# Kernel tuning notes

Measured on AMD Instinct MI355X. Metric: run time of the kernel, lower is better.

Reference implementation:

```python
import jax, jax.numpy as jnp
import numpy as np

B, S, D = 16, 2048, 1024
FF = 4 * D
ST, EN = 0, 512          # target_dims['start'], target_dims['end']
DT = EN - ST             # intervened subspace dim


def setup_inputs() -> dict:
    key = jax.random.key(0)
    k = jax.random.split(key, 6)
    hidden_states = jax.random.normal(k[0], (B, S, D), dtype=jnp.float32)
    eot_indices = jax.random.randint(k[1], (B,), 0, S)
    scale = 0.02
    W1 = jax.random.normal(k[2], (D, FF), dtype=jnp.float32) * scale
    W2 = jax.random.normal(k[3], (FF, D), dtype=jnp.float32) * scale
    W_rot = jax.random.normal(k[4], (DT, DT), dtype=jnp.float32) * scale
    W_inv = jax.random.normal(k[5], (DT, DT), dtype=jnp.float32) * scale
    return {"hidden_states": hidden_states, "W1": W1, "W2": W2,
            "W_rot": W_rot, "W_inv": W_inv, "eot_indices": eot_indices}


def reference(hidden_states, W1, W2, W_rot, W_inv, eot_indices):
    # layers[0]: transformer FFN block (stand-in for the wrapped encoder layer)
    h = jax.nn.gelu(hidden_states @ W1) @ W2          # [B, S, D]
    b = jnp.arange(h.shape[0])
    # LinearLayer branch: gather per-example eot row, slice target subspace
    rows = h[b, eot_indices]                          # [B, D]
    target = rows[:, ST:EN]                           # [B, DT]
    # LinearLayer -> InverseLinearLayer: rotate then un-rotate the subspace
    intervention = (target @ W_rot) @ W_inv           # [B, DT]
    # scatter/replace back into the flattened hidden states (vectorized form
    # of the per-example flatten/slice/cat/stack loop in the original code)
    new_rows = rows.at[:, ST:EN].set(intervention)    # [B, D]
    reps = h.at[b, eot_indices].set(new_rows)         # [B, S, D]
    return reps
```

## Files before the change

### kernel.cpp

```cpp
#include <hip/hip_runtime.h>
#include <hip/hip_bf16.h>
#include <stdint.h>

#define B_SZ  16
#define S_SZ  2048
#define D_SZ  1024
#define FF_SZ 4096
#define DT_SZ 512

typedef __bf16 bf16x8 __attribute__((ext_vector_type(8)));
typedef float  f32x4  __attribute__((ext_vector_type(4)));
typedef short  short8 __attribute__((ext_vector_type(8)));

__device__ __forceinline__ short f2bf(float x) {
    union { float f; uint32_t u; } v; v.f = x;
    uint32_t r = (v.u + 0x7fffu + ((v.u >> 16) & 1u)) >> 16;
    return (short)(uint16_t)r;
}

__global__ void cast_x_kernel(const float* __restrict__ src, short* __restrict__ dst, int n8) {
    int i = blockIdx.x * 256 + threadIdx.x;
    if (i >= n8) return;
    const float4* s4 = reinterpret_cast<const float4*>(src);
    float4 a = s4[2 * i], b = s4[2 * i + 1];
    short8 v;
    v[0] = f2bf(a.x); v[1] = f2bf(a.y); v[2] = f2bf(a.z); v[3] = f2bf(a.w);
    v[4] = f2bf(b.x); v[5] = f2bf(b.y); v[6] = f2bf(b.z); v[7] = f2bf(b.w);
    reinterpret_cast<short8*>(dst)[i] = v;
}

__global__ void transpose_cast_kernel(const float* __restrict__ src, short* __restrict__ dst,
                                      int R, int C) {
    __shared__ float tile[32][33];
    int c0 = blockIdx.x * 32, r0 = blockIdx.y * 32;
    int tx = threadIdx.x, ty = threadIdx.y;
#pragma unroll
    for (int i = 0; i < 32; i += 8)
        tile[ty + i][tx] = src[(size_t)(r0 + ty + i) * C + (c0 + tx)];
    __syncthreads();
#pragma unroll
    for (int i = 0; i < 32; i += 8)
        dst[(size_t)(c0 + ty + i) * R + (r0 + tx)] = f2bf(tile[tx][ty + i]);
}


#define GLOAD(srcp, dstofs)                                                   \
    __builtin_amdgcn_global_load_lds(                                         \
        (__attribute__((address_space(1))) void*)(srcp),                      \
        (__attribute__((address_space(3))) void*)(ldsb + (dstofs)), 16, 0, 0)

#define WSLOT(S) (((S) + 3) & 3)

#define TILE(S, NW, STG, TT) do {                                                           \
    asm volatile("s_waitcnt vmcnt(" #NW ")" ::: "memory");                                  \
    __builtin_amdgcn_s_barrier();                                                           \
    asm volatile("" ::: "memory");                                                          \
    __builtin_amdgcn_sched_barrier(0);                                                      \
    bf16x8 af0[4], af1[4], bfv[4];                                                          \
    _Pragma("unroll")                                                                       \
    for (int ni = 0; ni < 4; ++ni)                                                          \
        bfv[ni] = *reinterpret_cast<const bf16x8*>(ldsb + (S) * 32768 + offB[ni]);          \
    _Pragma("unroll")                                                                       \
    for (int mi = 0; mi < 4; ++mi)                                                          \
        af0[mi] = *reinterpret_cast<const bf16x8*>(ldsb + (S) * 32768 + offA[mi]);          \
    _Pragma("unroll")                                                                       \
    for (int mi = 0; mi < 4; ++mi)                                                          \
        af1[mi] = *reinterpret_cast<const bf16x8*>(ldsb + (S) * 32768 + offA[4 + mi]);      \
    if (STG) {                                                                              \
        GLOAD(gA0 + (size_t)(TT + 3) * 32, WSLOT(S) * 32768 +         w * 1024);            \
        GLOAD(gA1 + (size_t)(TT + 3) * 32, WSLOT(S) * 32768 +  8192 + w * 1024);            \
        GLOAD(gB0 + (size_t)(TT + 3) * 32, WSLOT(S) * 32768 + 16384 + w * 1024);            \
        GLOAD(gB1 + (size_t)(TT + 3) * 32, WSLOT(S) * 32768 + 24576 + w * 1024);            \
    }                                                                                       \
    __builtin_amdgcn_s_setprio(1);                                                          \
    _Pragma("unroll")                                                                       \
    for (int mi = 0; mi < 4; ++mi)                                                          \
        _Pragma("unroll")                                                                   \
        for (int ni = 0; ni < 4; ++ni)                                                      \
            acc[mi][ni] = __builtin_amdgcn_mfma_f32_16x16x32_bf16(af0[mi], bfv[ni],         \
                                                                  acc[mi][ni], 0, 0, 0);    \
    _Pragma("unroll")                                                                       \
    for (int mi = 0; mi < 4; ++mi)                                                          \
        _Pragma("unroll")                                                                   \
        for (int ni = 0; ni < 4; ++ni)                                                      \
            acc[4 + mi][ni] = __builtin_amdgcn_mfma_f32_16x16x32_bf16(af1[mi], bfv[ni],     \
                                                                  acc[4 + mi][ni], 0, 0, 0);\
    __builtin_amdgcn_s_setprio(0);                                                          \
} while (0)

template <bool GELU_BF16>
__global__ __launch_bounds__(512, 2)
void gemm256_kernel(const short* __restrict__ A, const short* __restrict__ Bt,
                    void* __restrict__ Cout, int M, int N, int K) {
    __shared__ char lds4[4][32768];
    char* ldsb = &lds4[0][0];

    const int tid = threadIdx.x;
    const int w   = tid >> 6;
    const int l   = tid & 63;
    const int wm  = w >> 2;
    const int wn  = w & 3;
    const int kq  = l >> 4;
    const int l15 = l & 15;

    const int nwg = gridDim.x;
    int swzw = blockIdx.x;
    if ((nwg & 7) == 0) swzw = (swzw & 7) * (nwg >> 3) + (swzw >> 3);
    const int MB = M >> 8;
    const int bm = swzw % MB, bn = swzw / MB;
    const int m0 = bm << 8, n0 = bn << 8;

    int offA[8], offB[4];
#pragma unroll
    for (int mi = 0; mi < 8; ++mi) {
        const int r = wm * 128 + mi * 16 + l15;
        offA[mi] = (r * 64 + kq * 16) ^ (((r >> 1) & 7) << 4);
    }
#pragma unroll
    for (int ni = 0; ni < 4; ++ni) {
        const int r = wn * 64 + ni * 16 + l15;
        offB[ni] = 16384 + ((r * 64 + kq * 16) ^ (((r >> 1) & 7) << 4));
    }

    const int X  = tid * 16;
    const int P  = X ^ (((X >> 7) & 7) << 4);
    const int rS = P >> 6;
    const int cS = (P & 63) >> 1;
    const short* gA0 = A  + (size_t)(m0 + rS) * K + cS;
    const short* gA1 = gA0 + (size_t)128 * K;
    const short* gB0 = Bt + (size_t)(n0 + rS) * K + cS;
    const short* gB1 = gB0 + (size_t)128 * K;

    f32x4 acc[8][4];
#pragma unroll
    for (int mi = 0; mi < 8; ++mi)
#pragma unroll
        for (int ni = 0; ni < 4; ++ni)
            acc[mi][ni] = (f32x4){0.f, 0.f, 0.f, 0.f};

    const int NT = K >> 5;

#pragma unroll
    for (int x = 0; x < 3; ++x) {
        GLOAD(gA0 + x * 32, x * 32768 +         w * 1024);
        GLOAD(gA1 + x * 32, x * 32768 +  8192 + w * 1024);
        GLOAD(gB0 + x * 32, x * 32768 + 16384 + w * 1024);
        GLOAD(gB1 + x * 32, x * 32768 + 24576 + w * 1024);
    }

    int t = 0;
    for (; t + 8 <= NT; t += 4) {
        TILE(0, 8, true, t);
        TILE(1, 8, true, t + 1);
        TILE(2, 8, true, t + 2);
        TILE(3, 8, true, t + 3);
    }
    TILE(0, 8, true,  t);
    TILE(1, 8, false, t + 1);
    TILE(2, 4, false, t + 2);
    TILE(3, 0, false, t + 3);

    const int row_base = m0 + wm * 128 + kq * 4;
    const int col_base = n0 + wn * 64 + l15;
    if constexpr (GELU_BF16) {
        short* C = reinterpret_cast<short*>(Cout);
#pragma unroll
        for (int mi = 0; mi < 8; ++mi)
#pragma unroll
            for (int r = 0; r < 4; ++r) {
                const size_t ro = (size_t)(row_base + mi * 16 + r) * N;
#pragma unroll
                for (int ni = 0; ni < 4; ++ni) {
                    float x = acc[mi][ni][r];
                    float u = 0.7978845608028654f * (x + 0.044715f * x * x * x);
                    float g = x / (1.f + __expf(-2.f * u));
                    C[ro + col_base + ni * 16] = f2bf(g);
                }
            }
    } else {
        float* C = reinterpret_cast<float*>(Cout);
#pragma unroll
        for (int mi = 0; mi < 8; ++mi)
#pragma unroll
            for (int r = 0; r < 4; ++r) {
                const size_t ro = (size_t)(row_base + mi * 16 + r) * N;
#pragma unroll
                for (int ni = 0; ni < 4; ++ni)
                    C[ro + col_base + ni * 16] = acc[mi][ni][r];
            }
    }
}

__global__ void intervention_kernel(const float* __restrict__ Wrot, const float* __restrict__ Winv,
                                    const int* __restrict__ eot, float* __restrict__ out) {
    __shared__ float tgt[DT_SZ];
    __shared__ float tmp[DT_SZ];
    const int b = blockIdx.x;
    const int j = threadIdx.x;
    float* row = out + ((size_t)b * S_SZ + eot[b]) * D_SZ;
    tgt[j] = row[j];
    __syncthreads();
    float s = 0.f;
#pragma unroll 8
    for (int i = 0; i < DT_SZ; ++i) s = fmaf(tgt[i], Wrot[(size_t)i * DT_SZ + j], s);
    tmp[j] = s;
    __syncthreads();
    float s2 = 0.f;
#pragma unroll 8
    for (int i = 0; i < DT_SZ; ++i) s2 = fmaf(tmp[i], Winv[(size_t)i * DT_SZ + j], s2);
    row[j] = s2;
}

extern "C" void kernel_launch(void* const* d_in, const int* in_sizes, int n_in,
                              void* d_out, int out_size, void* d_ws, size_t ws_size,
                              hipStream_t stream) {
    const float* hidden = (const float*)d_in[0];
    const float* W1     = (const float*)d_in[1];
    const float* W2     = (const float*)d_in[2];
    const float* Wrot   = (const float*)d_in[3];
    const float* Winv   = (const float*)d_in[4];
    const int*   eot    = (const int*)d_in[5];
    float* out = (float*)d_out;

    const int M = B_SZ * S_SZ;

    short* W1t = (short*)d_ws;
    short* W2t = W1t + (size_t)FF_SZ * D_SZ;
    short* Xbf = W2t + (size_t)FF_SZ * D_SZ;
    const size_t fixed_bytes = 2ull * (size_t)FF_SZ * D_SZ * sizeof(short);
    const size_t per_row = (size_t)D_SZ * 2 + (size_t)FF_SZ * 2;
    size_t rem = ws_size > fixed_bytes ? ws_size - fixed_bytes : 0;
    int Mc = (int)(rem / per_row);
    Mc = (Mc / 512) * 512;
    if (Mc < 512) Mc = 512;
    if (Mc > M) Mc = M;
    short* C1 = Xbf + (size_t)Mc * D_SZ;

    transpose_cast_kernel<<<dim3(FF_SZ / 32, D_SZ / 32), dim3(32, 8), 0, stream>>>(W1, W1t, D_SZ, FF_SZ);
    transpose_cast_kernel<<<dim3(D_SZ / 32, FF_SZ / 32), dim3(32, 8), 0, stream>>>(W2, W2t, FF_SZ, D_SZ);

    for (int ms = 0; ms < M; ms += Mc) {
        const int mc = (M - ms < Mc) ? (M - ms) : Mc;
        const int n8 = mc * D_SZ / 8;
        cast_x_kernel<<<(n8 + 255) / 256, 256, 0, stream>>>(hidden + (size_t)ms * D_SZ, Xbf, n8);
        gemm256_kernel<true ><<<dim3((mc / 256) * (FF_SZ / 256)), 512, 0, stream>>>(
            Xbf, W1t, C1, mc, FF_SZ, D_SZ);
        gemm256_kernel<false><<<dim3((mc / 256) * (D_SZ / 256)), 512, 0, stream>>>(
            C1, W2t, out + (size_t)ms * D_SZ, mc, D_SZ, FF_SZ);
    }
    intervention_kernel<<<B_SZ, DT_SZ, 0, stream>>>(Wrot, Winv, eot, out);
}
```

Measured before the change: 717.7 us.

## Double-buffer LDS fragment reads in registers to overlap with MFMA

Restructures the GEMM main loop so each iteration prefetches the next k-tile's A/B fragments from LDS into a second register set while MFMAs consume the current set. It waits on vmcnt for the next slot and uses lgkmcnt to let LDS reads run concurrently with math, hiding LDS latency. This doubles fragment register usage (24 more bf16x8 vectors per thread), which risks spills at the 512x2 launch bound. The vmcnt and barrier placement are retuned to match.

Measured after the change: 1.211 ms. 68.8% more time.

```diff
diff --git a/kernel.cpp b/kernel.cpp
--- a/kernel.cpp
+++ b/kernel.cpp
@@ -51,41 +51,36 @@
 
 #define WSLOT(S) (((S) + 3) & 3)
 
-#define TILE(S, NW, STG, TT) do {                                                           \
+#define TILE(S, P, NW, STG, RD, LG, TT) do {                                                \
     asm volatile("s_waitcnt vmcnt(" #NW ")" ::: "memory");                                  \
     __builtin_amdgcn_s_barrier();                                                           \
-    asm volatile("" ::: "memory");                                                          \
     __builtin_amdgcn_sched_barrier(0);                                                      \
-    bf16x8 af0[4], af1[4], bfv[4];                                                          \
-    _Pragma("unroll")                                                                       \
-    for (int ni = 0; ni < 4; ++ni)                                                          \
-        bfv[ni] = *reinterpret_cast<const bf16x8*>(ldsb + (S) * 32768 + offB[ni]);          \
-    _Pragma("unroll")                                                                       \
-    for (int mi = 0; mi < 4; ++mi)                                                          \
-        af0[mi] = *reinterpret_cast<const bf16x8*>(ldsb + (S) * 32768 + offA[mi]);          \
-    _Pragma("unroll")                                                                       \
-    for (int mi = 0; mi < 4; ++mi)                                                          \
-        af1[mi] = *reinterpret_cast<const bf16x8*>(ldsb + (S) * 32768 + offA[4 + mi]);      \
     if (STG) {                                                                              \
         GLOAD(gA0 + (size_t)(TT + 3) * 32, WSLOT(S) * 32768 +         w * 1024);            \
         GLOAD(gA1 + (size_t)(TT + 3) * 32, WSLOT(S) * 32768 +  8192 + w * 1024);            \
         GLOAD(gB0 + (size_t)(TT + 3) * 32, WSLOT(S) * 32768 + 16384 + w * 1024);            \
         GLOAD(gB1 + (size_t)(TT + 3) * 32, WSLOT(S) * 32768 + 24576 + w * 1024);            \
     }                                                                                       \
+    if (RD) {                                                                               \
+        const int ns_ = (((S) + 1) & 3) * 32768;                                            \
+        _Pragma("unroll")                                                                   \
+        for (int ni = 0; ni < 4; ++ni)                                                      \
+            bfvR[(P) ^ 1][ni] = *reinterpret_cast<const bf16x8*>(ldsb + ns_ + offB[ni]);    \
+        _Pragma("unroll")                                                                   \
+        for (int mi = 0; mi < 8; ++mi)                                                      \
+            afR[(P) ^ 1][mi] = *reinterpret_cast<const bf16x8*>(ldsb + ns_ + offA[mi]);     \
+    }                                                                                       \
+    asm volatile("s_waitcnt lgkmcnt(" #LG ")" ::: "memory");                                \
+    __builtin_amdgcn_sched_barrier(0);                                                      \
     __builtin_amdgcn_s_setprio(1);                                                          \
     _Pragma("unroll")                                                                       \
-    for (int mi = 0; mi < 4; ++mi)                                                          \
+    for (int mi = 0; mi < 8; ++mi)                                                          \
         _Pragma("unroll")                                                                   \
         for (int ni = 0; ni < 4; ++ni)                                                      \
-            acc[mi][ni] = __builtin_amdgcn_mfma_f32_16x16x32_bf16(af0[mi], bfv[ni],         \
+            acc[mi][ni] = __builtin_amdgcn_mfma_f32_16x16x32_bf16(afR[P][mi], bfvR[P][ni],  \
                                                                   acc[mi][ni], 0, 0, 0);    \
-    _Pragma("unroll")                                                                       \
-    for (int mi = 0; mi < 4; ++mi)                                                          \
-        _Pragma("unroll")                                                                   \
-        for (int ni = 0; ni < 4; ++ni)                                                      \
-            acc[4 + mi][ni] = __builtin_amdgcn_mfma_f32_16x16x32_bf16(af1[mi], bfv[ni],     \
-                                                                  acc[4 + mi][ni], 0, 0, 0);\
     __builtin_amdgcn_s_setprio(0);                                                          \
+    __builtin_amdgcn_sched_barrier(0);                                                      \
 } while (0)
 
 template <bool GELU_BF16>
@@ -138,6 +133,7 @@
         for (int ni = 0; ni < 4; ++ni)
             acc[mi][ni] = (f32x4){0.f, 0.f, 0.f, 0.f};
 
+    bf16x8 afR[2][8], bfvR[2][4];
     const int NT = K >> 5;
 
 #pragma unroll
@@ -147,18 +143,27 @@
         GLOAD(gB0 + x * 32, x * 32768 + 16384 + w * 1024);
         GLOAD(gB1 + x * 32, x * 32768 + 24576 + w * 1024);
     }
+    asm volatile("s_waitcnt vmcnt(8)" ::: "memory");
+    __builtin_amdgcn_s_barrier();
+    __builtin_amdgcn_sched_barrier(0);
+#pragma unroll
+    for (int ni = 0; ni < 4; ++ni)
+        bfvR[0][ni] = *reinterpret_cast<const bf16x8*>(ldsb + offB[ni]);
+#pragma unroll
+    for (int mi = 0; mi < 8; ++mi)
+        afR[0][mi] = *reinterpret_cast<const bf16x8*>(ldsb + offA[mi]);
 
     int t = 0;
     for (; t + 8 <= NT; t += 4) {
-        TILE(0, 8, true, t);
-        TILE(1, 8, true, t + 1);
-        TILE(2, 8, true, t + 2);
-        TILE(3, 8, true, t + 3);
-    }
-    TILE(0, 8, true,  t);
-    TILE(1, 8, false, t + 1);
-    TILE(2, 4, false, t + 2);
-    TILE(3, 0, false, t + 3);
+        TILE(0, 0, 4, 1, 1, 12, t);
+        TILE(1, 1, 4, 1, 1, 12, t + 1);
+        TILE(2, 0, 4, 1, 1, 12, t + 2);
+        TILE(3, 1, 4, 1, 1, 12, t + 3);
+    }
+    TILE(0, 0, 4, 1, 1, 12, t);
+    TILE(1, 1, 4, 0, 1, 12, t + 1);
+    TILE(2, 0, 0, 0, 1, 12, t + 2);
+    TILE(3, 1, 0, 0, 0, 0,  t + 3);
 
     const int row_base = m0 + wm * 128 + kq * 4;
     const int col_base = n0 + wn * 64 + l15;
```

## Restructure GEMM main loop into 8-phase ping-pong schedule with 64-wide K tiles

Applied to the files above, without the earlier changes.

Replaces the 4-slot, K=32 LDS ring buffer with a 2-slot, K=64 double buffer. Each K tile is now split into 8 phases that interleave half-tile global-to-LDS loads with MFMA groups, with barriers and waitcnts placed per phase. The LDS swizzle changes to a 128-byte row layout that XORs with the low row bits. The aim is finer overlap of memory traffic and MFMA work with fewer full-tile waits, at the cost of many more barriers and a different bank-conflict pattern in the new swizzle.

Measured after the change: 672.4 us. -6.3%, faster.

```diff
diff --git a/kernel.cpp b/kernel.cpp
--- a/kernel.cpp
+++ b/kernel.cpp
@@ -49,51 +49,78 @@
         (__attribute__((address_space(1))) void*)(srcp),                      \
         (__attribute__((address_space(3))) void*)(ldsb + (dstofs)), 16, 0, 0)
 
-#define WSLOT(S) (((S) + 3) & 3)
-
-#define TILE(S, NW, STG, TT) do {                                                           \
-    asm volatile("s_waitcnt vmcnt(" #NW ")" ::: "memory");                                  \
-    __builtin_amdgcn_s_barrier();                                                           \
-    asm volatile("" ::: "memory");                                                          \
-    __builtin_amdgcn_sched_barrier(0);                                                      \
-    bf16x8 af0[4], af1[4], bfv[4];                                                          \
-    _Pragma("unroll")                                                                       \
-    for (int ni = 0; ni < 4; ++ni)                                                          \
-        bfv[ni] = *reinterpret_cast<const bf16x8*>(ldsb + (S) * 32768 + offB[ni]);          \
+#define ABASE(S) ((S) * 65536)
+#define BBASE(S) ((S) * 65536 + 32768)
+
+#define STG_A(S, H, T) do {                                                                 \
+    GLOAD(gA[H][0] + (size_t)(T) * 64, ABASE(S) + (H) * 16384 +        w * 1024);           \
+    GLOAD(gA[H][1] + (size_t)(T) * 64, ABASE(S) + (H) * 16384 + 8192 + w * 1024);           \
+} while (0)
+#define STG_B(S, H, T) do {                                                                 \
+    GLOAD(gB[H][0] + (size_t)(T) * 64, BBASE(S) + (H) * 16384 +        w * 1024);           \
+    GLOAD(gB[H][1] + (size_t)(T) * 64, BBASE(S) + (H) * 16384 + 8192 + w * 1024);           \
+} while (0)
+#define NOSTG ((void)0)
+#define VM2  asm volatile("s_waitcnt vmcnt(2)" ::: "memory")
+#define VM0  asm volatile("s_waitcnt vmcnt(0)" ::: "memory")
+#define NOVM ((void)0)
+
+#define PHASE(S, KS, MIG, RB, VM, ...) do {                                                 \
+    if (RB) {                                                                               \
+        _Pragma("unroll")                                                                   \
+        for (int ni = 0; ni < 4; ++ni)                                                      \
+            bfv[ni] = *reinterpret_cast<const bf16x8*>(                                     \
+                ldsb + BBASE(S) + (offB[ni] ^ ((KS) * 64)));                                \
+    }                                                                                       \
     _Pragma("unroll")                                                                       \
     for (int mi = 0; mi < 4; ++mi)                                                          \
-        af0[mi] = *reinterpret_cast<const bf16x8*>(ldsb + (S) * 32768 + offA[mi]);          \
-    _Pragma("unroll")                                                                       \
-    for (int mi = 0; mi < 4; ++mi)                                                          \
-        af1[mi] = *reinterpret_cast<const bf16x8*>(ldsb + (S) * 32768 + offA[4 + mi]);      \
-    if (STG) {                                                                              \
-        GLOAD(gA0 + (size_t)(TT + 3) * 32, WSLOT(S) * 32768 +         w * 1024);            \
-        GLOAD(gA1 + (size_t)(TT + 3) * 32, WSLOT(S) * 32768 +  8192 + w * 1024);            \
-        GLOAD(gB0 + (size_t)(TT + 3) * 32, WSLOT(S) * 32768 + 16384 + w * 1024);            \
-        GLOAD(gB1 + (size_t)(TT + 3) * 32, WSLOT(S) * 32768 + 24576 + w * 1024);            \
-    }                                                                                       \
+        af[mi] = *reinterpret_cast<const bf16x8*>(                                          \
+            ldsb + ABASE(S) + (offA[(MIG) * 4 + mi] ^ ((KS) * 64)));                        \
+    __VA_ARGS__;                                                                            \
+    __builtin_amdgcn_s_barrier();                                                           \
+    asm volatile("s_waitcnt lgkmcnt(0)" ::: "memory");                                      \
+    __builtin_amdgcn_sched_barrier(0);                                                      \
     __builtin_amdgcn_s_setprio(1);                                                          \
     _Pragma("unroll")                                                                       \
     for (int mi = 0; mi < 4; ++mi)                                                          \
         _Pragma("unroll")                                                                   \
         for (int ni = 0; ni < 4; ++ni)                                                      \
-            acc[mi][ni] = __builtin_amdgcn_mfma_f32_16x16x32_bf16(af0[mi], bfv[ni],         \
-                                                                  acc[mi][ni], 0, 0, 0);    \
-    _Pragma("unroll")                                                                       \
-    for (int mi = 0; mi < 4; ++mi)                                                          \
-        _Pragma("unroll")                                                                   \
-        for (int ni = 0; ni < 4; ++ni)                                                      \
-            acc[4 + mi][ni] = __builtin_amdgcn_mfma_f32_16x16x32_bf16(af1[mi], bfv[ni],     \
-                                                                  acc[4 + mi][ni], 0, 0, 0);\
+            acc[(MIG) * 4 + mi][ni] = __builtin_amdgcn_mfma_f32_16x16x32_bf16(              \
+                af[mi], bfv[ni], acc[(MIG) * 4 + mi][ni], 0, 0, 0);                         \
     __builtin_amdgcn_s_setprio(0);                                                          \
+    __builtin_amdgcn_sched_barrier(0);                                                      \
+    VM;                                                                                     \
+    __builtin_amdgcn_s_barrier();                                                           \
+} while (0)
+
+#define ITER_FULL(T) do {                                                                   \
+    PHASE(0, 0, 0, 1, NOVM, STG_B(1, 1, (T) + 1));                                          \
+    PHASE(0, 0, 1, 0, NOVM, STG_A(1, 0, (T) + 1));                                          \
+    PHASE(0, 1, 0, 1, NOVM, STG_A(1, 1, (T) + 1));                                          \
+    PHASE(0, 1, 1, 0, VM2,  STG_B(0, 0, (T) + 2));                                          \
+    PHASE(1, 0, 0, 1, NOVM, STG_B(0, 1, (T) + 2));                                          \
+    PHASE(1, 0, 1, 0, NOVM, STG_A(0, 0, (T) + 2));                                          \
+    PHASE(1, 1, 0, 1, NOVM, STG_A(0, 1, (T) + 2));                                          \
+    PHASE(1, 1, 1, 0, VM2,  STG_B(1, 0, (T) + 3));                                          \
+} while (0)
+
+#define ITER_LAST(T) do {                                                                   \
+    PHASE(0, 0, 0, 1, NOVM, STG_B(1, 1, (T) + 1));                                          \
+    PHASE(0, 0, 1, 0, NOVM, STG_A(1, 0, (T) + 1));                                          \
+    PHASE(0, 1, 0, 1, NOVM, STG_A(1, 1, (T) + 1));                                          \
+    PHASE(0, 1, 1, 0, VM0,  NOSTG);                                                         \
+    PHASE(1, 0, 0, 1, NOVM, NOSTG);                                                         \
+    PHASE(1, 0, 1, 0, NOVM, NOSTG);                                                         \
+    PHASE(1, 1, 0, 1, NOVM, NOSTG);                                                         \
+    PHASE(1, 1, 1, 0, NOVM, NOSTG);                                                         \
 } while (0)
 
 template <bool GELU_BF16>
 __global__ __launch_bounds__(512, 2)
 void gemm256_kernel(const short* __restrict__ A, const short* __restrict__ Bt,
                     void* __restrict__ Cout, int M, int N, int K) {
-    __shared__ char lds4[4][32768];
-    char* ldsb = &lds4[0][0];
+    __shared__ char lds2[2][65536];
+    char* ldsb = &lds2[0][0];
 
     const int tid = threadIdx.x;
     const int w   = tid >> 6;
@@ -114,22 +141,25 @@
 #pragma unroll
     for (int mi = 0; mi < 8; ++mi) {
         const int r = wm * 128 + mi * 16 + l15;
-        offA[mi] = (r * 64 + kq * 16) ^ (((r >> 1) & 7) << 4);
+        offA[mi] = r * 128 + ((kq ^ (r & 7)) << 4);
     }
 #pragma unroll
     for (int ni = 0; ni < 4; ++ni) {
         const int r = wn * 64 + ni * 16 + l15;
-        offB[ni] = 16384 + ((r * 64 + kq * 16) ^ (((r >> 1) & 7) << 4));
-    }
-
-    const int X  = tid * 16;
-    const int P  = X ^ (((X >> 7) & 7) << 4);
-    const int rS = P >> 6;
-    const int cS = (P & 63) >> 1;
-    const short* gA0 = A  + (size_t)(m0 + rS) * K + cS;
-    const short* gA1 = gA0 + (size_t)128 * K;
-    const short* gB0 = Bt + (size_t)(n0 + rS) * K + cS;
-    const short* gB1 = gB0 + (size_t)128 * K;
+        offB[ni] = r * 128 + ((kq ^ (r & 7)) << 4);
+    }
+
+    const short *gA[2][2], *gB[2][2];
+#pragma unroll
+    for (int h = 0; h < 2; ++h)
+#pragma unroll
+        for (int j = 0; j < 2; ++j) {
+            const int X = tid * 16 + j * 8192;
+            const int P = X ^ (((X >> 7) & 7) << 4);
+            const int r = P >> 7, c = (P & 127) >> 1;
+            gA[h][j] = A  + (size_t)(m0 + h * 128 + r) * K + c;
+            gB[h][j] = Bt + (size_t)(n0 + h * 128 + r) * K + c;
+        }
 
     f32x4 acc[8][4];
 #pragma unroll
@@ -138,27 +168,23 @@
         for (int ni = 0; ni < 4; ++ni)
             acc[mi][ni] = (f32x4){0.f, 0.f, 0.f, 0.f};
 
-    const int NT = K >> 5;
-
-#pragma unroll
-    for (int x = 0; x < 3; ++x) {
-        GLOAD(gA0 + x * 32, x * 32768 +         w * 1024);
-        GLOAD(gA1 + x * 32, x * 32768 +  8192 + w * 1024);
-        GLOAD(gB0 + x * 32, x * 32768 + 16384 + w * 1024);
-        GLOAD(gB1 + x * 32, x * 32768 + 24576 + w * 1024);
-    }
-
-    int t = 0;
-    for (; t + 8 <= NT; t += 4) {
-        TILE(0, 8, true, t);
-        TILE(1, 8, true, t + 1);
-        TILE(2, 8, true, t + 2);
-        TILE(3, 8, true, t + 3);
-    }
-    TILE(0, 8, true,  t);
-    TILE(1, 8, false, t + 1);
-    TILE(2, 4, false, t + 2);
-    TILE(3, 0, false, t + 3);
+    bf16x8 af[4], bfv[4];
+    const int NT = K >> 6;
+    const int NI = NT >> 1;
+
+    STG_B(0, 0, 0);
+    STG_B(0, 1, 0);
+    STG_A(0, 0, 0);
+    STG_A(0, 1, 0);
+    STG_B(1, 0, 1);
+    VM2;
+    __builtin_amdgcn_s_barrier();
+
+    for (int i = 0; i < NI - 1; ++i) {
+        const int T = 2 * i;
+        ITER_FULL(T);
+    }
+    ITER_LAST(2 * (NI - 1));
 
     const int row_base = m0 + wm * 128 + kq * 4;
     const int col_base = n0 + wn * 64 + l15;
```

## Switch GEMM to 32x32x16 MFMA with BK=64 double-buffered LDS pipeline

Applied to the files above, without the earlier changes.

Rewrites the bf16 GEMM main loop to use 32x32x16 MFMA instructions instead of 16x16x32, with each K step widened to 64. It replaces the 4-slot, 3-ahead global-to-LDS pipeline with a 2-slot double buffer that waits on all outstanding loads each step, and reorders block mapping to be row-major over N. The aim is fewer LDS fragment reads per FLOP and better MFMA efficiency. In exchange there is less prefetch depth for hiding memory latency, and the s_setprio hints are dropped.

Result: no change. 722.5 us (+0.7%).

```diff
diff --git a/kernel.cpp b/kernel.cpp
--- a/kernel.cpp
+++ b/kernel.cpp
@@ -9,7 +9,7 @@
 #define DT_SZ 512
 
 typedef __bf16 bf16x8 __attribute__((ext_vector_type(8)));
-typedef float  f32x4  __attribute__((ext_vector_type(4)));
+typedef float  f32x16 __attribute__((ext_vector_type(16)));
 typedef short  short8 __attribute__((ext_vector_type(8)));
 
 __device__ __forceinline__ short f2bf(float x) {
@@ -49,145 +49,132 @@
         (__attribute__((address_space(1))) void*)(srcp),                      \
         (__attribute__((address_space(3))) void*)(ldsb + (dstofs)), 16, 0, 0)
 
-#define WSLOT(S) (((S) + 3) & 3)
-
-#define TILE(S, NW, STG, TT) do {                                                           \
-    asm volatile("s_waitcnt vmcnt(" #NW ")" ::: "memory");                                  \
+#define STAGE(S, T) do {                                                                    \
+    _Pragma("unroll")                                                                       \
+    for (int j = 0; j < 4; ++j)                                                             \
+        GLOAD(gA[j] + (size_t)(T) * 64, (S) * 65536 +         j * 8192 + tid * 16);         \
+    _Pragma("unroll")                                                                       \
+    for (int j = 0; j < 4; ++j)                                                             \
+        GLOAD(gB[j] + (size_t)(T) * 64, (S) * 65536 + 32768 + j * 8192 + tid * 16);         \
+} while (0)
+
+#define STEP(S, T, STG) do {                                                                \
+    asm volatile("s_waitcnt vmcnt(0)" ::: "memory");                                        \
     __builtin_amdgcn_s_barrier();                                                           \
-    asm volatile("" ::: "memory");                                                          \
+    if (STG) STAGE((S) ^ 1, (T) + 1);                                                       \
     __builtin_amdgcn_sched_barrier(0);                                                      \
-    bf16x8 af0[4], af1[4], bfv[4];                                                          \
     _Pragma("unroll")                                                                       \
-    for (int ni = 0; ni < 4; ++ni)                                                          \
-        bfv[ni] = *reinterpret_cast<const bf16x8*>(ldsb + (S) * 32768 + offB[ni]);          \
-    _Pragma("unroll")                                                                       \
-    for (int mi = 0; mi < 4; ++mi)                                                          \
-        af0[mi] = *reinterpret_cast<const bf16x8*>(ldsb + (S) * 32768 + offA[mi]);          \
-    _Pragma("unroll")                                                                       \
-    for (int mi = 0; mi < 4; ++mi)                                                          \
-        af1[mi] = *reinterpret_cast<const bf16x8*>(ldsb + (S) * 32768 + offA[4 + mi]);      \
-    if (STG) {                                                                              \
-        GLOAD(gA0 + (size_t)(TT + 3) * 32, WSLOT(S) * 32768 +         w * 1024);            \
-        GLOAD(gA1 + (size_t)(TT + 3) * 32, WSLOT(S) * 32768 +  8192 + w * 1024);            \
-        GLOAD(gB0 + (size_t)(TT + 3) * 32, WSLOT(S) * 32768 + 16384 + w * 1024);            \
-        GLOAD(gB1 + (size_t)(TT + 3) * 32, WSLOT(S) * 32768 + 24576 + w * 1024);            \
+    for (int ks = 0; ks < 4; ++ks) {                                                        \
+        bf16x8 a[4], b[2];                                                                  \
+        _Pragma("unroll")                                                                   \
+        for (int mi = 0; mi < 4; ++mi)                                                      \
+            a[mi] = *reinterpret_cast<const bf16x8*>(                                       \
+                ldsb + (S) * 65536 + (offA0[mi] ^ (ks << 5)));                              \
+        _Pragma("unroll")                                                                   \
+        for (int ni = 0; ni < 2; ++ni)                                                      \
+            b[ni] = *reinterpret_cast<const bf16x8*>(                                       \
+                ldsb + (S) * 65536 + (offB0[ni] ^ (ks << 5)));                              \
+        _Pragma("unroll")                                                                   \
+        for (int mi = 0; mi < 4; ++mi)                                                      \
+            _Pragma("unroll")                                                               \
+            for (int ni = 0; ni < 2; ++ni)                                                  \
+                acc[mi][ni] = __builtin_amdgcn_mfma_f32_32x32x16_bf16(                      \
+                    a[mi], b[ni], acc[mi][ni], 0, 0, 0);                                    \
     }                                                                                       \
-    __builtin_amdgcn_s_setprio(1);                                                          \
-    _Pragma("unroll")                                                                       \
-    for (int mi = 0; mi < 4; ++mi)                                                          \
-        _Pragma("unroll")                                                                   \
-        for (int ni = 0; ni < 4; ++ni)                                                      \
-            acc[mi][ni] = __builtin_amdgcn_mfma_f32_16x16x32_bf16(af0[mi], bfv[ni],         \
-                                                                  acc[mi][ni], 0, 0, 0);    \
-    _Pragma("unroll")                                                                       \
-    for (int mi = 0; mi < 4; ++mi)                                                          \
-        _Pragma("unroll")                                                                   \
-        for (int ni = 0; ni < 4; ++ni)                                                      \
-            acc[4 + mi][ni] = __builtin_amdgcn_mfma_f32_16x16x32_bf16(af1[mi], bfv[ni],     \
-                                                                  acc[4 + mi][ni], 0, 0, 0);\
-    __builtin_amdgcn_s_setprio(0);                                                          \
 } while (0)
 
 template <bool GELU_BF16>
 __global__ __launch_bounds__(512, 2)
 void gemm256_kernel(const short* __restrict__ A, const short* __restrict__ Bt,
                     void* __restrict__ Cout, int M, int N, int K) {
-    __shared__ char lds4[4][32768];
-    char* ldsb = &lds4[0][0];
+    __shared__ char lds2[2][65536];
+    char* ldsb = &lds2[0][0];
 
     const int tid = threadIdx.x;
     const int w   = tid >> 6;
     const int l   = tid & 63;
     const int wm  = w >> 2;
     const int wn  = w & 3;
-    const int kq  = l >> 4;
-    const int l15 = l & 15;
+    const int l31 = l & 31;
+    const int lh  = l >> 5;
 
     const int nwg = gridDim.x;
     int swzw = blockIdx.x;
     if ((nwg & 7) == 0) swzw = (swzw & 7) * (nwg >> 3) + (swzw >> 3);
-    const int MB = M >> 8;
-    const int bm = swzw % MB, bn = swzw / MB;
+    const int NB = N >> 8;
+    const int bm = swzw / NB, bn = swzw % NB;
     const int m0 = bm << 8, n0 = bn << 8;
 
-    int offA[8], offB[4];
-#pragma unroll
-    for (int mi = 0; mi < 8; ++mi) {
-        const int r = wm * 128 + mi * 16 + l15;
-        offA[mi] = (r * 64 + kq * 16) ^ (((r >> 1) & 7) << 4);
-    }
-#pragma unroll
-    for (int ni = 0; ni < 4; ++ni) {
-        const int r = wn * 64 + ni * 16 + l15;
-        offB[ni] = 16384 + ((r * 64 + kq * 16) ^ (((r >> 1) & 7) << 4));
-    }
-
-    const int X  = tid * 16;
-    const int P  = X ^ (((X >> 7) & 7) << 4);
-    const int rS = P >> 6;
-    const int cS = (P & 63) >> 1;
-    const short* gA0 = A  + (size_t)(m0 + rS) * K + cS;
-    const short* gA1 = gA0 + (size_t)128 * K;
-    const short* gB0 = Bt + (size_t)(n0 + rS) * K + cS;
-    const short* gB1 = gB0 + (size_t)128 * K;
-
-    f32x4 acc[8][4];
-#pragma unroll
-    for (int mi = 0; mi < 8; ++mi)
-#pragma unroll
-        for (int ni = 0; ni < 4; ++ni)
-            acc[mi][ni] = (f32x4){0.f, 0.f, 0.f, 0.f};
-
-    const int NT = K >> 5;
-
-#pragma unroll
-    for (int x = 0; x < 3; ++x) {
-        GLOAD(gA0 + x * 32, x * 32768 +         w * 1024);
-        GLOAD(gA1 + x * 32, x * 32768 +  8192 + w * 1024);
-        GLOAD(gB0 + x * 32, x * 32768 + 16384 + w * 1024);
-        GLOAD(gB1 + x * 32, x * 32768 + 24576 + w * 1024);
-    }
-
-    int t = 0;
-    for (; t + 8 <= NT; t += 4) {
-        TILE(0, 8, true, t);
-        TILE(1, 8, true, t + 1);
-        TILE(2, 8, true, t + 2);
-        TILE(3, 8, true, t + 3);
-    }
-    TILE(0, 8, true,  t);
-    TILE(1, 8, false, t + 1);
-    TILE(2, 4, false, t + 2);
-    TILE(3, 0, false, t + 3);
-
-    const int row_base = m0 + wm * 128 + kq * 4;
-    const int col_base = n0 + wn * 64 + l15;
+    int offA0[4], offB0[2];
+#pragma unroll
+    for (int mi = 0; mi < 4; ++mi) {
+        const int r = wm * 128 + mi * 32 + l31;
+        offA0[mi] = r * 128 + ((lh ^ (r & 7)) << 4);
+    }
+#pragma unroll
+    for (int ni = 0; ni < 2; ++ni) {
+        const int r = wn * 64 + ni * 32 + l31;
+        offB0[ni] = 32768 + r * 128 + ((lh ^ (r & 7)) << 4);
+    }
+
+    const short *gA[4], *gB[4];
+#pragma unroll
+    for (int j = 0; j < 4; ++j) {
+        const int X = j * 8192 + tid * 16;
+        const int P = X ^ (((X >> 7) & 7) << 4);
+        const int r = P >> 7, c = (P & 127) >> 1;
+        gA[j] = A  + (size_t)(m0 + r) * K + c;
+        gB[j] = Bt + (size_t)(n0 + r) * K + c;
+    }
+
+    f32x16 acc[4][2];
+#pragma unroll
+    for (int mi = 0; mi < 4; ++mi)
+#pragma unroll
+        for (int ni = 0; ni < 2; ++ni)
+            acc[mi][ni] = (f32x16)(0.f);
+
+    const int NT = K >> 6;
+
+    STAGE(0, 0);
+
+    for (int t = 0; t < NT - 2; t += 2) {
+        STEP(0, t, 1);
+        STEP(1, t + 1, 1);
+    }
+    STEP(0, NT - 2, 1);
+    STEP(1, NT - 1, 0);
+
+    const int col0 = n0 + wn * 64 + l31;
     if constexpr (GELU_BF16) {
         short* C = reinterpret_cast<short*>(Cout);
 #pragma unroll
-        for (int mi = 0; mi < 8; ++mi)
-#pragma unroll
-            for (int r = 0; r < 4; ++r) {
-                const size_t ro = (size_t)(row_base + mi * 16 + r) * N;
-#pragma unroll
-                for (int ni = 0; ni < 4; ++ni) {
-                    float x = acc[mi][ni][r];
+        for (int mi = 0; mi < 4; ++mi) {
+            const int rb = m0 + wm * 128 + mi * 32 + 4 * lh;
+#pragma unroll
+            for (int ni = 0; ni < 2; ++ni)
+#pragma unroll
+                for (int reg = 0; reg < 16; ++reg) {
+                    const int row = rb + (reg & 3) + 8 * (reg >> 2);
+                    float x = acc[mi][ni][reg];
                     float u = 0.7978845608028654f * (x + 0.044715f * x * x * x);
                     float g = x / (1.f + __expf(-2.f * u));
-                    C[ro + col_base + ni * 16] = f2bf(g);
+                    C[(size_t)row * N + col0 + ni * 32] = f2bf(g);
                 }
-            }
+        }
     } else {
         float* C = reinterpret_cast<float*>(Cout);
 #pragma unroll
-        for (int mi = 0; mi < 8; ++mi)
-#pragma unroll
-            for (int r = 0; r < 4; ++r) {
-                const size_t ro = (size_t)(row_base + mi * 16 + r) * N;
-#pragma unroll
-                for (int ni = 0; ni < 4; ++ni)
-                    C[ro + col_base + ni * 16] = acc[mi][ni][r];
-            }
+        for (int mi = 0; mi < 4; ++mi) {
+            const int rb = m0 + wm * 128 + mi * 32 + 4 * lh;
+#pragma unroll
+            for (int ni = 0; ni < 2; ++ni)
+#pragma unroll
+                for (int reg = 0; reg < 16; ++reg) {
+                    const int row = rb + (reg & 3) + 8 * (reg >> 2);
+                    C[(size_t)row * N + col0 + ni * 32] = acc[mi][ni][reg];
+                }
+        }
     }
 }
 
```
